# Performance work log

Hardware: AMD Instinct MI355X
Metric: run time of the kernel (lower is better)

## Reference

```python
import jax, jax.numpy as jnp
import numpy as np

N = 100000        # nodes
E = 1600000       # edges (avg in-degree 16)
D_IN = 128
H = 4             # num_heads
D = 16            # out_feats per head
NEG_SLOPE = 0.2


def setup_inputs() -> dict:
    key = jax.random.key(0)
    k1, k2, k3, k4, k5 = jax.random.split(key, 5)
    feat = jax.random.normal(k1, (N, D_IN), dtype=jnp.float32)
    src = jax.random.randint(k2, (E,), 0, N, dtype=jnp.int32)
    dst = jax.random.randint(k3, (E,), 0, N, dtype=jnp.int32)
    # learned parameters (xavier-ish scale)
    W = jax.random.normal(k4, (H * D, D_IN), dtype=jnp.float32) * (2.0 / np.sqrt(D_IN + H * D))
    attn_weights = jax.random.normal(k5, (2 * H * D,), dtype=jnp.float32) * 0.1
    bias = jnp.zeros((H * D,), dtype=jnp.float32)
    return {"feat": feat, "src": src, "dst": dst, "W": W,
            "attn_weights": attn_weights, "bias": bias}


def reference(feat, src, dst, W, attn_weights, bias):
    # linear projection: [N, H*D] -> [N, H, D]
    z = (feat @ W.T).reshape(N, H, D)
    a = attn_weights.reshape(2, H, D)
    # per-node attention logits for source/destination roles: [N, H]
    el = jnp.einsum('nhd,hd->nh', z, a[0])
    er = jnp.einsum('nhd,hd->nh', z, a[1])
    # per-edge logits + LeakyReLU: [E, H]
    e = jax.nn.leaky_relu(el[src] + er[dst], NEG_SLOPE)
    # segment softmax over incoming edges of each destination node
    m = jax.ops.segment_max(e, dst, num_segments=N)        # [N, H]
    m = jnp.where(jnp.isfinite(m), m, 0.0)                 # guard isolated nodes
    ex = jnp.exp(e - m[dst])                               # [E, H]
    denom = jax.ops.segment_sum(ex, dst, num_segments=N)   # [N, H]
    denom = jnp.where(denom > 0, denom, 1.0)
    alpha = ex / denom[dst]                                # [E, H]
    # weighted scatter-aggregate: out[dst] += alpha * z[src]
    out = jax.ops.segment_sum(alpha[:, :, None] * z[src], dst, num_segments=N)
    return out + bias.reshape(H, D)
```

## Files before the change

kernel.cpp:

```cpp
#include <hip/hip_runtime.h>
#include <hip/hip_fp16.h>
#include <math.h>

#define NUM_H 4
#define HD 64
#define DIN 128
#define NEG_SLOPE 0.2f
#define LOG2E 1.4426950408889634f

#define NBK 512
#define BSH 8
#define NCH 256
#define SEGS 2
#define CPS (NCH / SEGS)
#define SRCB 17

typedef _Float16 half8 __attribute__((ext_vector_type(8)));
typedef float f32x4 __attribute__((ext_vector_type(4)));

__device__ inline half8 pack8(float4 a, float4 b) {
  half8 h;
  h[0] = (_Float16)a.x; h[1] = (_Float16)a.y;
  h[2] = (_Float16)a.z; h[3] = (_Float16)a.w;
  h[4] = (_Float16)b.x; h[5] = (_Float16)b.y;
  h[6] = (_Float16)b.z; h[7] = (_Float16)b.w;
  return h;
}

__global__ __launch_bounds__(256) void k_hist(const int* __restrict__ dst,
                                              int* __restrict__ mat, int e) {
  __shared__ int h[NBK];
  for (int i = threadIdx.x; i < NBK; i += 256) h[i] = 0;
  __syncthreads();
  const int chunk = (e + NCH - 1) / NCH;
  const int lo = blockIdx.x * chunk;
  const int hi = min(e, lo + chunk);
  const int lo4 = min(hi, (lo + 3) & ~3);
  const int hi4 = (hi & ~3) < lo4 ? lo4 : (hi & ~3);
  for (int i = lo + threadIdx.x; i < lo4; i += 256)
    atomicAdd(&h[dst[i] >> BSH], 1);
  for (int i = lo4 + threadIdx.x * 4; i < hi4; i += 1024) {
    int4 d4 = *reinterpret_cast<const int4*>(dst + i);
    atomicAdd(&h[d4.x >> BSH], 1);
    atomicAdd(&h[d4.y >> BSH], 1);
    atomicAdd(&h[d4.z >> BSH], 1);
    atomicAdd(&h[d4.w >> BSH], 1);
  }
  for (int i = hi4 + threadIdx.x; i < hi; i += 256)
    atomicAdd(&h[dst[i] >> BSH], 1);
  __syncthreads();
  for (int i = threadIdx.x; i < NBK; i += 256)
    mat[blockIdx.x * NBK + i] = h[i];
}

__global__ __launch_bounds__(1024) void k_scanb(int* __restrict__ mat,
                                                int* __restrict__ segpre,
                                                int* __restrict__ bbase,
                                                int* __restrict__ offs,
                                                int e, int n) {
  __shared__ int part[SEGS][NBK];
  __shared__ int tot[NBK];
  const int t = threadIdx.x;
  const int b = t & (NBK - 1);
  const int seg = t >> 9;
  int run = 0;
  for (int c = seg * CPS; c < seg * CPS + CPS; ++c) {
    int v = mat[c * NBK + b];
    mat[c * NBK + b] = run;
    run += v;
  }
  part[seg][b] = run;
  __syncthreads();
  int mytot = 0;
  if (t < NBK) {
    int acc = 0;
#pragma unroll
    for (int s2 = 0; s2 < SEGS; ++s2) {
      segpre[s2 * NBK + b] = acc;
      acc += part[s2][b];
    }
    tot[b] = acc;
    mytot = acc;
  }
  __syncthreads();
  for (int off = 1; off < NBK; off <<= 1) {
    int x = 0;
    if (t < NBK && b >= off) x = tot[b - off];
    __syncthreads();
    if (t < NBK) tot[b] += x;
    __syncthreads();
  }
  if (t < NBK) {
    bbase[t] = tot[t] - mytot;
    if (t == NBK - 1) bbase[NBK] = tot[t];
    if (t == 0) offs[n] = e;
  }
}

__global__ __launch_bounds__(256) void k_proj_bucket(
    const float* __restrict__ feat, const float* __restrict__ Wm,
    const float* __restrict__ attn, const int* __restrict__ src,
    const int* __restrict__ dst, const int* __restrict__ mat,
    const int* __restrict__ segpre, const int* __restrict__ bbase,
    __half* __restrict__ zh, float* __restrict__ el, float* __restrict__ er,
    int* __restrict__ bkt, int n, int e) {
  __shared__ int cur[NBK];
  if ((int)blockIdx.x < NCH) {
    const int cb = blockIdx.x;
    const int seg = cb / CPS;
    for (int i = threadIdx.x; i < NBK; i += 256)
      cur[i] = bbase[i] + segpre[seg * NBK + i] + mat[cb * NBK + i];
    __syncthreads();
    const int chunk = (e + NCH - 1) / NCH;
    const int lo = cb * chunk;
    const int hi = min(e, lo + chunk);
    const int lo4 = min(hi, (lo + 3) & ~3);
    const int hi4 = (hi & ~3) < lo4 ? lo4 : (hi & ~3);
    for (int i = lo + threadIdx.x; i < lo4; i += 256) {
      int d = dst[i];
      int p = atomicAdd(&cur[d >> BSH], 1);
      bkt[p] = ((d & ((1 << BSH) - 1)) << SRCB) | src[i];
    }
    for (int i = lo4 + threadIdx.x * 4; i < hi4; i += 1024) {
      int4 d4 = *reinterpret_cast<const int4*>(dst + i);
      int4 s4 = *reinterpret_cast<const int4*>(src + i);
      int p0 = atomicAdd(&cur[d4.x >> BSH], 1);
      bkt[p0] = ((d4.x & ((1 << BSH) - 1)) << SRCB) | s4.x;
      int p1 = atomicAdd(&cur[d4.y >> BSH], 1);
      bkt[p1] = ((d4.y & ((1 << BSH) - 1)) << SRCB) | s4.y;
      int p2 = atomicAdd(&cur[d4.z >> BSH], 1);
      bkt[p2] = ((d4.z & ((1 << BSH) - 1)) << SRCB) | s4.z;
      int p3 = atomicAdd(&cur[d4.w >> BSH], 1);
      bkt[p3] = ((d4.w & ((1 << BSH) - 1)) << SRCB) | s4.w;
    }
    for (int i = hi4 + threadIdx.x; i < hi; i += 256) {
      int d = dst[i];
      int p = atomicAdd(&cur[d >> BSH], 1);
      bkt[p] = ((d & ((1 << BSH) - 1)) << SRCB) | src[i];
    }
    return;
  }

  const int pb = (int)blockIdx.x - NCH;
  const int lane = threadIdx.x & 63;
  const int wv = threadIdx.x >> 6;
  const int l15 = lane & 15;
  const int g = lane >> 4;
  const int base = pb * 64 + wv * 16;

  half8 bf[4][4];
#pragma unroll
  for (int j = 0; j < 4; ++j) {
    const float* wp = Wm + (j * 16 + l15) * 128 + g * 8;
#pragma unroll
    for (int kt = 0; kt < 4; ++kt) {
      float4 w0 = *(const float4*)(wp + kt * 32);
      float4 w1 = *(const float4*)(wp + kt * 32 + 4);
      bf[kt][j] = pack8(w0, w1);
    }
  }

  int arow = base + l15;
  if (arow > n - 1) arow = n - 1;
  const float* fp = feat + (size_t)arow * 128 + g * 8;
  half8 af[4];
#pragma unroll
  for (int kt = 0; kt < 4; ++kt) {
    float4 a0 = *(const float4*)(fp + kt * 32);
    float4 a1 = *(const float4*)(fp + kt * 32 + 4);
    af[kt] = pack8(a0, a1);
  }

  f32x4 acc[4] = {{0.f,0.f,0.f,0.f},{0.f,0.f,0.f,0.f},
                  {0.f,0.f,0.f,0.f},{0.f,0.f,0.f,0.f}};
#pragma unroll
  for (int kt = 0; kt < 4; ++kt)
#pragma unroll
    for (int j = 0; j < 4; ++j)
      acc[j] = __builtin_amdgcn_mfma_f32_16x16x32_f16(af[kt], bf[kt][j], acc[j], 0, 0, 0);

  float a0v[4], a1v[4];
#pragma unroll
  for (int j = 0; j < 4; ++j) {
    a0v[j] = attn[j * 16 + l15];
    a1v[j] = attn[64 + j * 16 + l15];
  }
#pragma unroll
  for (int r = 0; r < 4; ++r) {
    int row = base + g * 4 + r;
    bool ok = row < n;
#pragma unroll
    for (int j = 0; j < 4; ++j) {
      float v = acc[j][r];
      if (ok) zh[(size_t)row * 64 + j * 16 + l15] = __float2half_rn(v);
      float pl = v * a0v[j];
      float pr = v * a1v[j];
#pragma unroll
      for (int o = 8; o >= 1; o >>= 1) {
        pl += __shfl_xor(pl, o, 16);
        pr += __shfl_xor(pr, o, 16);
      }
      if (ok && l15 == 0) {
        el[row * 4 + j] = pl * LOG2E;
        er[row * 4 + j] = pr * LOG2E;
      }
    }
  }
}

__global__ __launch_bounds__(256) void k_csr(
    const int* __restrict__ bkt, const int* __restrict__ bbase,
    int* __restrict__ offs, int* __restrict__ csr, int n) {
  __shared__ int h[1 << BSH];
  __shared__ int pre[1 << BSH];
  const int b = blockIdx.x;
  const int base = bbase[b];
  const int cnt = bbase[b + 1] - base;
  const int nlo = b << BSH;
  const int t = threadIdx.x;

  h[t] = 0;
  __syncthreads();
  for (int i = t; i < cnt; i += 256)
    atomicAdd(&h[bkt[base + i] >> SRCB], 1);
  __syncthreads();

  int v = h[t];
  pre[t] = v;
  __syncthreads();
  for (int off = 1; off < 256; off <<= 1) {
    int x = (t >= off) ? pre[t - off] : 0;
    __syncthreads();
    pre[t] += x;
    __syncthreads();
  }
  int excl = pre[t] - v;
  if (nlo + t < n) offs[nlo + t] = base + excl;
  h[t] = excl;
  __syncthreads();
  for (int i = t; i < cnt; i += 256) {
    int w = bkt[base + i];
    int p = atomicAdd(&h[w >> SRCB], 1);
    csr[base + p] = w & ((1 << SRCB) - 1);
  }
}

__global__ __launch_bounds__(256) void k_gat(
    const __half2* __restrict__ zh, const float* __restrict__ el,
    const float* __restrict__ er, const int* __restrict__ offs,
    const int* __restrict__ csr, const float* __restrict__ bias,
    float* __restrict__ out, int n, int nwaves) {
  const int lane = threadIdx.x & 63;
  const int h = lane >> 4;
  const int slot = (lane >> 3) & 1;
  const int dp = lane & 7;
  const int gw = (blockIdx.x * 256 + threadIdx.x) >> 6;

  const float2 b2 = reinterpret_cast<const float2*>(bias)[h * 8 + dp];

  for (int node = gw; node < n; node += nwaves) {
    const int beg = offs[node], end = offs[node + 1];
    const float erh = er[node * 4 + h];
    float den = 0.f, ax = 0.f, ay = 0.f;

    int pb = beg;
    for (; pb + 8 <= end; pb += 8) {
      int q = pb + slot;
      int s0 = csr[q];
      int s1 = csr[q + 2];
      int s2 = csr[q + 4];
      int s3 = csr[q + 6];
      float x0 = el[s0 * 4 + h] + erh;
      float x1 = el[s1 * 4 + h] + erh;
      float x2 = el[s2 * 4 + h] + erh;
      float x3 = el[s3 * 4 + h] + erh;
      x0 = fmaxf(x0, x0 * NEG_SLOPE);
      x1 = fmaxf(x1, x1 * NEG_SLOPE);
      x2 = fmaxf(x2, x2 * NEG_SLOPE);
      x3 = fmaxf(x3, x3 * NEG_SLOPE);
      float e0 = __builtin_amdgcn_exp2f(x0);
      float e1 = __builtin_amdgcn_exp2f(x1);
      float e2 = __builtin_amdgcn_exp2f(x2);
      float e3 = __builtin_amdgcn_exp2f(x3);
      float2 z0 = __half22float2(zh[s0 * 32 + h * 8 + dp]);
      float2 z1 = __half22float2(zh[s1 * 32 + h * 8 + dp]);
      float2 z2 = __half22float2(zh[s2 * 32 + h * 8 + dp]);
      float2 z3 = __half22float2(zh[s3 * 32 + h * 8 + dp]);
      den += e0 + e1 + e2 + e3;
      ax += e0 * z0.x + e1 * z1.x + e2 * z2.x + e3 * z3.x;
      ay += e0 * z0.y + e1 * z1.y + e2 * z2.y + e3 * z3.y;
    }
    for (int q = pb + slot; q < end; q += 2) {
      int s0 = csr[q];
      float x0 = el[s0 * 4 + h] + erh;
      x0 = fmaxf(x0, x0 * NEG_SLOPE);
      float e0 = __builtin_amdgcn_exp2f(x0);
      float2 z0 = __half22float2(zh[s0 * 32 + h * 8 + dp]);
      den += e0;
      ax += e0 * z0.x;
      ay += e0 * z0.y;
    }

    den += __shfl_xor(den, 8);
    ax += __shfl_xor(ax, 8);
    ay += __shfl_xor(ay, 8);
    if (slot == 0) {
      float d = den <= 0.f ? 1.f : den;
      float inv = 1.f / d;
      float2 o2 = make_float2(ax * inv + b2.x, ay * inv + b2.y);
      reinterpret_cast<float2*>(out)[node * 32 + h * 8 + dp] = o2;
    }
  }
}

extern "C" void kernel_launch(void* const* d_in, const int* in_sizes, int n_in,
                              void* d_out, int out_size, void* d_ws, size_t ws_size,
                              hipStream_t stream) {
  const float* feat = (const float*)d_in[0];
  const int* src = (const int*)d_in[1];
  const int* dst = (const int*)d_in[2];
  const float* Wm = (const float*)d_in[3];
  const float* attn = (const float*)d_in[4];
  const float* bias = (const float*)d_in[5];
  const int n = in_sizes[0] / DIN;
  const int e = in_sizes[1];
  float* out = (float*)d_out;

  __half* zh = (__half*)d_ws;
  int* bkt = (int*)(zh + (size_t)n * HD);
  float* el = (float*)(bkt + e);
  float* er = el + (size_t)n * NUM_H;
  int* offs = (int*)(er + (size_t)n * NUM_H);
  int* csr = offs + (n + 1);
  int* mat = csr + e;
  int* segpre = mat + NCH * NBK;
  int* bbase = segpre + SEGS * NBK;

  const int PB = (n + 63) / 64;
  k_hist<<<NCH, 256, 0, stream>>>(dst, mat, e);
  k_scanb<<<1, 1024, 0, stream>>>(mat, segpre, bbase, offs, e, n);
  k_proj_bucket<<<NCH + PB, 256, 0, stream>>>(feat, Wm, attn, src, dst, mat,
                                              segpre, bbase, zh, el, er, bkt,
                                              n, e);
  int nbuckets = (n + (1 << BSH) - 1) >> BSH;
  k_csr<<<nbuckets, 256, 0, stream>>>(bkt, bbase, offs, csr, n);
  const int GB = 2048;
  k_gat<<<GB, 256, 0, stream>>>((const __half2*)zh, el, er, offs, csr, bias,
                                out, n, GB * 4);
}
```

Before: 141.8 us.

## Fuse projection with histogram and transpose count matrix for vectorized scan

The feature projection now runs alongside the edge histogram in one launch, and the bucket scatter becomes its own kernel. The per-chunk count matrix is stored transposed (bucket-major), so the single-block scan reads and writes each thread's contiguous row with int4 accesses instead of strided scalar ones. The aim is to shorten the serial scan and keep the projection work off the critical path between scan and scatter. In exchange, the standalone bucket kernel has only 256 blocks, so nothing else runs alongside it to fill the GPU.

```diff
diff --git a/kernel.cpp b/kernel.cpp
--- a/kernel.cpp
+++ b/kernel.cpp
@@ -27,30 +27,103 @@
   return h;
 }
 
-__global__ __launch_bounds__(256) void k_hist(const int* __restrict__ dst,
-                                              int* __restrict__ mat, int e) {
-  __shared__ int h[NBK];
-  for (int i = threadIdx.x; i < NBK; i += 256) h[i] = 0;
-  __syncthreads();
-  const int chunk = (e + NCH - 1) / NCH;
-  const int lo = blockIdx.x * chunk;
-  const int hi = min(e, lo + chunk);
-  const int lo4 = min(hi, (lo + 3) & ~3);
-  const int hi4 = (hi & ~3) < lo4 ? lo4 : (hi & ~3);
-  for (int i = lo + threadIdx.x; i < lo4; i += 256)
-    atomicAdd(&h[dst[i] >> BSH], 1);
-  for (int i = lo4 + threadIdx.x * 4; i < hi4; i += 1024) {
-    int4 d4 = *reinterpret_cast<const int4*>(dst + i);
-    atomicAdd(&h[d4.x >> BSH], 1);
-    atomicAdd(&h[d4.y >> BSH], 1);
-    atomicAdd(&h[d4.z >> BSH], 1);
-    atomicAdd(&h[d4.w >> BSH], 1);
-  }
-  for (int i = hi4 + threadIdx.x; i < hi; i += 256)
-    atomicAdd(&h[dst[i] >> BSH], 1);
-  __syncthreads();
-  for (int i = threadIdx.x; i < NBK; i += 256)
-    mat[blockIdx.x * NBK + i] = h[i];
+__global__ __launch_bounds__(256) void k_proj_hist(
+    const float* __restrict__ feat, const float* __restrict__ Wm,
+    const float* __restrict__ attn, const int* __restrict__ dst,
+    __half* __restrict__ zh, float* __restrict__ el, float* __restrict__ er,
+    int* __restrict__ mat, int n, int e, int PB) {
+  __shared__ int hsh[NBK];
+  if ((int)blockIdx.x >= PB) {
+    const int cb = (int)blockIdx.x - PB;
+    for (int i = threadIdx.x; i < NBK; i += 256) hsh[i] = 0;
+    __syncthreads();
+    const int chunk = (e + NCH - 1) / NCH;
+    const int lo = cb * chunk;
+    const int hi = min(e, lo + chunk);
+    const int lo4 = min(hi, (lo + 3) & ~3);
+    const int hi4 = (hi & ~3) < lo4 ? lo4 : (hi & ~3);
+    for (int i = lo + threadIdx.x; i < lo4; i += 256)
+      atomicAdd(&hsh[dst[i] >> BSH], 1);
+    for (int i = lo4 + threadIdx.x * 4; i < hi4; i += 1024) {
+      int4 d4 = *reinterpret_cast<const int4*>(dst + i);
+      atomicAdd(&hsh[d4.x >> BSH], 1);
+      atomicAdd(&hsh[d4.y >> BSH], 1);
+      atomicAdd(&hsh[d4.z >> BSH], 1);
+      atomicAdd(&hsh[d4.w >> BSH], 1);
+    }
+    for (int i = hi4 + threadIdx.x; i < hi; i += 256)
+      atomicAdd(&hsh[dst[i] >> BSH], 1);
+    __syncthreads();
+    for (int i = threadIdx.x; i < NBK; i += 256)
+      mat[i * NCH + cb] = hsh[i];
+    return;
+  }
+
+  const int pb = blockIdx.x;
+  const int lane = threadIdx.x & 63;
+  const int wv = threadIdx.x >> 6;
+  const int l15 = lane & 15;
+  const int g = lane >> 4;
+  const int base = pb * 64 + wv * 16;
+
+  half8 bf[4][4];
+#pragma unroll
+  for (int j = 0; j < 4; ++j) {
+    const float* wp = Wm + (j * 16 + l15) * 128 + g * 8;
+#pragma unroll
+    for (int kt = 0; kt < 4; ++kt) {
+      float4 w0 = *(const float4*)(wp + kt * 32);
+      float4 w1 = *(const float4*)(wp + kt * 32 + 4);
+      bf[kt][j] = pack8(w0, w1);
+    }
+  }
+
+  int arow = base + l15;
+  if (arow > n - 1) arow = n - 1;
+  const float* fp = feat + (size_t)arow * 128 + g * 8;
+  half8 af[4];
+#pragma unroll
+  for (int kt = 0; kt < 4; ++kt) {
+    float4 a0 = *(const float4*)(fp + kt * 32);
+    float4 a1 = *(const float4*)(fp + kt * 32 + 4);
+    af[kt] = pack8(a0, a1);
+  }
+
+  f32x4 acc[4] = {{0.f,0.f,0.f,0.f},{0.f,0.f,0.f,0.f},
+                  {0.f,0.f,0.f,0.f},{0.f,0.f,0.f,0.f}};
+#pragma unroll
+  for (int kt = 0; kt < 4; ++kt)
+#pragma unroll
+    for (int j = 0; j < 4; ++j)
+      acc[j] = __builtin_amdgcn_mfma_f32_16x16x32_f16(af[kt], bf[kt][j], acc[j], 0, 0, 0);
+
+  float a0v[4], a1v[4];
+#pragma unroll
+  for (int j = 0; j < 4; ++j) {
+    a0v[j] = attn[j * 16 + l15];
+    a1v[j] = attn[64 + j * 16 + l15];
+  }
+#pragma unroll
+  for (int r = 0; r < 4; ++r) {
+    int row = base + g * 4 + r;
+    bool ok = row < n;
+#pragma unroll
+    for (int j = 0; j < 4; ++j) {
+      float v = acc[j][r];
+      if (ok) zh[(size_t)row * 64 + j * 16 + l15] = __float2half_rn(v);
+      float pl = v * a0v[j];
+      float pr = v * a1v[j];
+#pragma unroll
+      for (int o = 8; o >= 1; o >>= 1) {
+        pl += __shfl_xor(pl, o, 16);
+        pr += __shfl_xor(pr, o, 16);
+      }
+      if (ok && l15 == 0) {
+        el[row * 4 + j] = pl * LOG2E;
+        er[row * 4 + j] = pr * LOG2E;
+      }
+    }
+  }
 }
 
 __global__ __launch_bounds__(1024) void k_scanb(int* __restrict__ mat,
@@ -63,11 +136,25 @@
   const int t = threadIdx.x;
   const int b = t & (NBK - 1);
   const int seg = t >> 9;
+  const int c0 = b * NCH + seg * CPS;
   int run = 0;
-  for (int c = seg * CPS; c < seg * CPS + CPS; ++c) {
-    int v = mat[c * NBK + b];
-    mat[c * NBK + b] = run;
-    run += v;
+#pragma unroll
+  for (int r = 0; r < CPS / 32; ++r) {
+    int4 v4[8];
+#pragma unroll
+    for (int k = 0; k < 8; ++k)
+      v4[k] = *reinterpret_cast<const int4*>(&mat[c0 + r * 32 + k * 4]);
+#pragma unroll
+    for (int k = 0; k < 8; ++k) {
+      int a = v4[k].x, bb = v4[k].y, cc = v4[k].z, dd = v4[k].w;
+      v4[k].x = run; run += a;
+      v4[k].y = run; run += bb;
+      v4[k].z = run; run += cc;
+      v4[k].w = run; run += dd;
+    }
+#pragma unroll
+    for (int k = 0; k < 8; ++k)
+      *reinterpret_cast<int4*>(&mat[c0 + r * 32 + k * 4]) = v4[k];
   }
   part[seg][b] = run;
   __syncthreads();
@@ -97,114 +184,42 @@
   }
 }
 
-__global__ __launch_bounds__(256) void k_proj_bucket(
-    const float* __restrict__ feat, const float* __restrict__ Wm,
-    const float* __restrict__ attn, const int* __restrict__ src,
-    const int* __restrict__ dst, const int* __restrict__ mat,
-    const int* __restrict__ segpre, const int* __restrict__ bbase,
-    __half* __restrict__ zh, float* __restrict__ el, float* __restrict__ er,
-    int* __restrict__ bkt, int n, int e) {
+__global__ __launch_bounds__(256) void k_bucket(
+    const int* __restrict__ src, const int* __restrict__ dst,
+    const int* __restrict__ mat, const int* __restrict__ segpre,
+    const int* __restrict__ bbase, int* __restrict__ bkt, int e) {
   __shared__ int cur[NBK];
-  if ((int)blockIdx.x < NCH) {
-    const int cb = blockIdx.x;
-    const int seg = cb / CPS;
-    for (int i = threadIdx.x; i < NBK; i += 256)
-      cur[i] = bbase[i] + segpre[seg * NBK + i] + mat[cb * NBK + i];
-    __syncthreads();
-    const int chunk = (e + NCH - 1) / NCH;
-    const int lo = cb * chunk;
-    const int hi = min(e, lo + chunk);
-    const int lo4 = min(hi, (lo + 3) & ~3);
-    const int hi4 = (hi & ~3) < lo4 ? lo4 : (hi & ~3);
-    for (int i = lo + threadIdx.x; i < lo4; i += 256) {
-      int d = dst[i];
-      int p = atomicAdd(&cur[d >> BSH], 1);
-      bkt[p] = ((d & ((1 << BSH) - 1)) << SRCB) | src[i];
-    }
-    for (int i = lo4 + threadIdx.x * 4; i < hi4; i += 1024) {
-      int4 d4 = *reinterpret_cast<const int4*>(dst + i);
-      int4 s4 = *reinterpret_cast<const int4*>(src + i);
-      int p0 = atomicAdd(&cur[d4.x >> BSH], 1);
-      bkt[p0] = ((d4.x & ((1 << BSH) - 1)) << SRCB) | s4.x;
-      int p1 = atomicAdd(&cur[d4.y >> BSH], 1);
-      bkt[p1] = ((d4.y & ((1 << BSH) - 1)) << SRCB) | s4.y;
-      int p2 = atomicAdd(&cur[d4.z >> BSH], 1);
-      bkt[p2] = ((d4.z & ((1 << BSH) - 1)) << SRCB) | s4.z;
-      int p3 = atomicAdd(&cur[d4.w >> BSH], 1);
-      bkt[p3] = ((d4.w & ((1 << BSH) - 1)) << SRCB) | s4.w;
-    }
-    for (int i = hi4 + threadIdx.x; i < hi; i += 256) {
-      int d = dst[i];
-      int p = atomicAdd(&cur[d >> BSH], 1);
-      bkt[p] = ((d & ((1 << BSH) - 1)) << SRCB) | src[i];
-    }
-    return;
-  }
-
-  const int pb = (int)blockIdx.x - NCH;
-  const int lane = threadIdx.x & 63;
-  const int wv = threadIdx.x >> 6;
-  const int l15 = lane & 15;
-  const int g = lane >> 4;
-  const int base = pb * 64 + wv * 16;
-
-  half8 bf[4][4];
-#pragma unroll
-  for (int j = 0; j < 4; ++j) {
-    const float* wp = Wm + (j * 16 + l15) * 128 + g * 8;
-#pragma unroll
-    for (int kt = 0; kt < 4; ++kt) {
-      float4 w0 = *(const float4*)(wp + kt * 32);
-      float4 w1 = *(const float4*)(wp + kt * 32 + 4);
-      bf[kt][j] = pack8(w0, w1);
-    }
-  }
-
-  int arow = base + l15;
-  if (arow > n - 1) arow = n - 1;
-  const float* fp = feat + (size_t)arow * 128 + g * 8;
-  half8 af[4];
-#pragma unroll
-  for (int kt = 0; kt < 4; ++kt) {
-    float4 a0 = *(const float4*)(fp + kt * 32);
-    float4 a1 = *(const float4*)(fp + kt * 32 + 4);
-    af[kt] = pack8(a0, a1);
-  }
-
-  f32x4 acc[4] = {{0.f,0.f,0.f,0.f},{0.f,0.f,0.f,0.f},
-                  {0.f,0.f,0.f,0.f},{0.f,0.f,0.f,0.f}};
-#pragma unroll
-  for (int kt = 0; kt < 4; ++kt)
-#pragma unroll
-    for (int j = 0; j < 4; ++j)
-      acc[j] = __builtin_amdgcn_mfma_f32_16x16x32_f16(af[kt], bf[kt][j], acc[j], 0, 0, 0);
-
-  float a0v[4], a1v[4];
-#pragma unroll
-  for (int j = 0; j < 4; ++j) {
-    a0v[j] = attn[j * 16 + l15];
-    a1v[j] = attn[64 + j * 16 + l15];
-  }
-#pragma unroll
-  for (int r = 0; r < 4; ++r) {
-    int row = base + g * 4 + r;
-    bool ok = row < n;
-#pragma unroll
-    for (int j = 0; j < 4; ++j) {
-      float v = acc[j][r];
-      if (ok) zh[(size_t)row * 64 + j * 16 + l15] = __float2half_rn(v);
-      float pl = v * a0v[j];
-      float pr = v * a1v[j];
-#pragma unroll
-      for (int o = 8; o >= 1; o >>= 1) {
-        pl += __shfl_xor(pl, o, 16);
-        pr += __shfl_xor(pr, o, 16);
-      }
-      if (ok && l15 == 0) {
-        el[row * 4 + j] = pl * LOG2E;
-        er[row * 4 + j] = pr * LOG2E;
-      }
-    }
+  const int cb = blockIdx.x;
+  const int seg = cb / CPS;
+  for (int i = threadIdx.x; i < NBK; i += 256)
+    cur[i] = bbase[i] + segpre[seg * NBK + i] + mat[i * NCH + cb];
+  __syncthreads();
+  const int chunk = (e + NCH - 1) / NCH;
+  const int lo = cb * chunk;
+  const int hi = min(e, lo + chunk);
+  const int lo4 = min(hi, (lo + 3) & ~3);
+  const int hi4 = (hi & ~3) < lo4 ? lo4 : (hi & ~3);
+  for (int i = lo + threadIdx.x; i < lo4; i += 256) {
+    int d = dst[i];
+    int p = atomicAdd(&cur[d >> BSH], 1);
+    bkt[p] = ((d & ((1 << BSH) - 1)) << SRCB) | src[i];
+  }
+  for (int i = lo4 + threadIdx.x * 4; i < hi4; i += 1024) {
+    int4 d4 = *reinterpret_cast<const int4*>(dst + i);
+    int4 s4 = *reinterpret_cast<const int4*>(src + i);
+    int p0 = atomicAdd(&cur[d4.x >> BSH], 1);
+    bkt[p0] = ((d4.x & ((1 << BSH) - 1)) << SRCB) | s4.x;
+    int p1 = atomicAdd(&cur[d4.y >> BSH], 1);
+    bkt[p1] = ((d4.y & ((1 << BSH) - 1)) << SRCB) | s4.y;
+    int p2 = atomicAdd(&cur[d4.z >> BSH], 1);
+    bkt[p2] = ((d4.z & ((1 << BSH) - 1)) << SRCB) | s4.z;
+    int p3 = atomicAdd(&cur[d4.w >> BSH], 1);
+    bkt[p3] = ((d4.w & ((1 << BSH) - 1)) << SRCB) | s4.w;
+  }
+  for (int i = hi4 + threadIdx.x; i < hi; i += 256) {
+    int d = dst[i];
+    int p = atomicAdd(&cur[d >> BSH], 1);
+    bkt[p] = ((d & ((1 << BSH) - 1)) << SRCB) | src[i];
   }
 }
 
@@ -333,15 +348,14 @@
   int* offs = (int*)(er + (size_t)n * NUM_H);
   int* csr = offs + (n + 1);
   int* mat = csr + e;
-  int* segpre = mat + NCH * NBK;
+  int* segpre = mat + NBK * NCH;
   int* bbase = segpre + SEGS * NBK;
 
   const int PB = (n + 63) / 64;
-  k_hist<<<NCH, 256, 0, stream>>>(dst, mat, e);
+  k_proj_hist<<<PB + NCH, 256, 0, stream>>>(feat, Wm, attn, dst, zh, el, er,
+                                            mat, n, e, PB);
   k_scanb<<<1, 1024, 0, stream>>>(mat, segpre, bbase, offs, e, n);
-  k_proj_bucket<<<NCH + PB, 256, 0, stream>>>(feat, Wm, attn, src, dst, mat,
-                                              segpre, bbase, zh, el, er, bkt,
-                                              n, e);
+  k_bucket<<<NCH, 256, 0, stream>>>(src, dst, mat, segpre, bbase, bkt, e);
   int nbuckets = (n + (1 << BSH) - 1) >> BSH;
   k_csr<<<nbuckets, 256, 0, stream>>>(bkt, bbase, offs, csr, n);
   const int GB = 2048;
```

New measurement: 167.2 us. 1.18x slower.
